# Kernel optimization log

Hardware: AMD Instinct MI355X
Metric: run time of the kernel (lower is better)

The kernel has to match this reference:

```python
import jax, jax.numpy as jnp
import numpy as np

BS = 2
EMBED = 256
NH = 8
NL = 4
NP = 4
HD = EMBED // NH
SHAPES = [(128, 128), (64, 64), (32, 32), (16, 16)]
NQ = sum(h * w for h, w in SHAPES)  # 21760


def setup_inputs() -> dict:
    key = jax.random.key(0)
    ks = jax.random.split(key, 12)
    s = 1.0 / np.sqrt(EMBED)
    return {
        "query": jax.random.normal(ks[0], (BS, NQ, EMBED), jnp.float32),
        "reference_points": jax.random.uniform(ks[1], (BS, NQ, NL, 2), jnp.float32),
        "value": jax.random.normal(ks[2], (BS, NQ, EMBED), jnp.float32),
        "W_off": jax.random.normal(ks[3], (EMBED, NH * NL * NP * 2), jnp.float32) * 0.01,
        "b_off": jax.random.normal(ks[4], (NH * NL * NP * 2,), jnp.float32) * 0.5,
        "W_attn": jax.random.normal(ks[5], (EMBED, NH * NL * NP), jnp.float32) * 0.02,
        "b_attn": jnp.zeros((NH * NL * NP,), jnp.float32),
        "W_v": jax.random.normal(ks[6], (EMBED, EMBED), jnp.float32) * s,
        "b_v": jnp.zeros((EMBED,), jnp.float32),
        "W_out": jax.random.normal(ks[7], (EMBED, EMBED), jnp.float32) * s,
        "b_out": jnp.zeros((EMBED,), jnp.float32),
        "value_spatial_shapes": np.asarray(SHAPES, dtype=np.int64),
    }


def _ms_deform_attn(value, shapes, loc, aw):
    # value: [bs,V,nh,d]; loc: [bs,nq,nh,L,P,2] in [0,1]; aw: [bs,nq,nh,L,P]
    bs, V, nh, d = value.shape
    nq = loc.shape[1]
    out = jnp.zeros((bs, nq, nh, d), value.dtype)
    start = 0
    b_idx = jnp.arange(bs)[:, None, None, None]
    h_idx = jnp.arange(nh)[None, None, :, None]
    for l, (H, W) in enumerate(shapes):
        H, W = int(H), int(W)
        v = value[:, start:start + H * W].reshape(bs, H, W, nh, d)
        start += H * W
        g = 2.0 * loc[:, :, :, l] - 1.0  # [bs,nq,nh,P,2], grid_sample convention
        # align_corners=False pixel coordinates
        x = ((g[..., 0] + 1.0) * W - 1.0) * 0.5
        y = ((g[..., 1] + 1.0) * H - 1.0) * 0.5
        x0 = jnp.floor(x); y0 = jnp.floor(y)
        wx1 = x - x0; wx0 = 1.0 - wx1
        wy1 = y - y0; wy0 = 1.0 - wy1

        def gather(yi, xi):
            inb = (yi >= 0) & (yi < H) & (xi >= 0) & (xi < W)
            yc = jnp.clip(yi, 0, H - 1).astype(jnp.int32)
            xc = jnp.clip(xi, 0, W - 1).astype(jnp.int32)
            vals = v[b_idx, yc, xc, h_idx]  # [bs,nq,nh,P,d]
            return vals * inb[..., None].astype(v.dtype)

        samp = (gather(y0, x0) * (wy0 * wx0)[..., None]
                + gather(y0, x0 + 1) * (wy0 * wx1)[..., None]
                + gather(y0 + 1, x0) * (wy1 * wx0)[..., None]
                + gather(y0 + 1, x0 + 1) * (wy1 * wx1)[..., None])
        out = out + jnp.einsum('bqhpd,bqhp->bqhd', samp, aw[:, :, :, l])
    return out.reshape(bs, nq, nh * d)


def reference(query, reference_points, value, W_off, b_off, W_attn, b_attn,
              W_v, b_v, W_out, b_out, value_spatial_shapes):
    shapes = np.asarray(value_spatial_shapes)  # static [L,2]
    bs, nq, _ = query.shape
    v = (value @ W_v + b_v).reshape(bs, -1, NH, HD)
    off = (query @ W_off + b_off).reshape(bs, nq, NH, NL, NP, 2)
    aw = (query @ W_attn + b_attn).reshape(bs, nq, NH, NL * NP)
    aw = jax.nn.softmax(aw, axis=-1).reshape(bs, nq, NH, NL, NP)
    # offset normalizer: (W,H) per level
    norm = jnp.asarray(shapes[:, ::-1].astype(np.float32))  # [L,2]
    loc = reference_points[:, :, None, :, None, :] + off / norm[None, None, None, :, None, :]
    out = _ms_deform_attn(v, shapes, loc, aw)
    return out @ W_out + b_out
```

## Files before the change

### kernel.cpp

```cpp
#include <hip/hip_runtime.h>
#include <math.h>

#define BS 2
#define NQ 21760
#define V_LEN 21760
#define EMBED 256
#define NH 8
#define NL 4
#define NP 4
#define HD 32

typedef __bf16 bf16;
typedef __bf16 bf16x8 __attribute__((ext_vector_type(8)));
typedef __bf16 bf16x4 __attribute__((ext_vector_type(4)));
typedef float f32x4 __attribute__((ext_vector_type(4)));
typedef float f32x2 __attribute__((ext_vector_type(2)));
typedef unsigned int u32;

#define GLOAD_LDS16(gp, lp_) \
    __builtin_amdgcn_global_load_lds( \
        (const __attribute__((address_space(1))) unsigned int*)(gp), \
        (__attribute__((address_space(3))) unsigned int*)(lp_), 16, 0, 0)

__global__ __launch_bounds__(256) void cast_all(
    const float* __restrict__ W_v, const float* __restrict__ W_off,
    const float* __restrict__ W_attn, const float* __restrict__ W_out,
    const float* __restrict__ b_off, const float* __restrict__ b_attn,
    bf16* __restrict__ WTv, bf16* __restrict__ WToa, bf16* __restrict__ WTu,
    float* __restrict__ bcat)
{
    const int bid = blockIdx.x;
    const int tid = threadIdx.x;
    if (bid == 56) {
        if (tid < 384) bcat[tid] = (tid < 256) ? b_off[tid] : b_attn[tid - 256];
        return;
    }
    const float* W; bf16* WT; int N, tile;
    if (bid < 16)      { W = W_v;    WT = WTv;           N = 256; tile = bid; }
    else if (bid < 32) { W = W_off;  WT = WToa;          N = 256; tile = bid - 16; }
    else if (bid < 40) { W = W_attn; WT = WToa + 65536;  N = 128; tile = bid - 32; }
    else               { W = W_out;  WT = WTu;           N = 256; tile = bid - 40; }
    const int ntn = N >> 6;
    const int k0 = (tile / ntn) * 64, n0 = (tile % ntn) * 64;

    __shared__ float lds[64][65];
    const int c = tid & 63, r4 = tid >> 6;
    #pragma unroll
    for (int p = 0; p < 16; p++) {
        int rr = r4 + p * 4;
        lds[rr][c] = W[(size_t)(k0 + rr) * N + n0 + c];
    }
    __syncthreads();
    #pragma unroll
    for (int p = 0; p < 16; p++) {
        int i = r4 + p * 4;
        WT[(size_t)(n0 + i) * 256 + k0 + c] = (bf16)lds[c][i];
    }
}

template<bool A_F32, bool OUT_BF16>
__global__ __launch_bounds__(256) void gemm_mfma(
    const void* __restrict__ Av, const bf16* __restrict__ WT,
    const float* __restrict__ bias, void* __restrict__ Cv,
    int N, int K, int ntn)
{
    const int nmt = gridDim.x / ntn;
    const int bmt = blockIdx.x % nmt;
    const int bnt = blockIdx.x / nmt;
    const int bm = bmt * 128, bn = bnt * 128;

    __shared__ __align__(16) bf16 Bs[2][128 * 32];
    __shared__ __align__(16) unsigned char AsRaw[2][A_F32 ? 128 * 32 * 4
                                                         : 128 * 32 * 2];

    const int tid = threadIdx.x;
    const int lane = tid & 63, wv = tid >> 6;
    const int wr = wv >> 1, wc = wv & 1;
    const int quad = lane >> 4, l16 = lane & 15;

    f32x4 acc[4][4];
    #pragma unroll
    for (int i = 0; i < 4; i++)
        #pragma unroll
        for (int j = 0; j < 4; j++)
            acc[i][j] = (f32x4){0.f, 0.f, 0.f, 0.f};

    const int b_row = tid >> 2, b_chunk = tid & 3;
    const int a_row8 = tid >> 3, a_phys = tid & 7;
    constexpr int NB = A_F32 ? 6 : 4;

    auto stage = [&](int buf, int k0) {
        if constexpr (A_F32) {
            const float* A = (const float*)Av;
            #pragma unroll
            for (int p = 0; p < 4; p++) {
                int row = a_row8 + p * 32;
                int csrc = a_phys ^ (row & 7);
                GLOAD_LDS16(&A[(size_t)(bm + row) * K + k0 + csrc * 4],
                            &AsRaw[buf][p * 4096 + tid * 16]);
            }
        } else {
            const bf16* A = (const bf16*)Av;
            #pragma unroll
            for (int p = 0; p < 2; p++) {
                int row = b_row + p * 64;
                GLOAD_LDS16(&A[(size_t)(bm + row) * K + k0 + b_chunk * 8],
                            &AsRaw[buf][p * 4096 + tid * 16]);
            }
        }
        #pragma unroll
        for (int p = 0; p < 2; p++) {
            int row = b_row + p * 64;
            GLOAD_LDS16(&WT[(size_t)(bn + row) * K + k0 + b_chunk * 8],
                        (unsigned char*)&Bs[buf][0] + p * 4096 + tid * 16);
        }
    };

    const int nt = K >> 5;
    stage(0, 0);
    int cur = 0;
    for (int t = 0; t < nt; t++) {
        __builtin_amdgcn_s_barrier();
        if (t + 1 < nt) {
            stage(cur ^ 1, (t + 1) << 5);
            asm volatile("s_waitcnt vmcnt(%0)" :: "n"(NB) : "memory");
        } else {
            asm volatile("s_waitcnt vmcnt(0)" ::: "memory");
        }
        __builtin_amdgcn_s_barrier();

        bf16x8 af[4], bfr[4];
        if constexpr (A_F32) {
            const float* Asf = (const float*)&AsRaw[cur][0];
            #pragma unroll
            for (int mi = 0; mi < 4; mi++) {
                int r = wr * 64 + mi * 16 + l16;
                int g = r & 7;
                f32x4 u0 = *(const f32x4*)&Asf[r * 32 + ((2 * quad) ^ g) * 4];
                f32x4 u1 = *(const f32x4*)&Asf[r * 32 + ((2 * quad + 1) ^ g) * 4];
                bf16x8 hh;
                hh[0] = (bf16)u0[0]; hh[1] = (bf16)u0[1]; hh[2] = (bf16)u0[2]; hh[3] = (bf16)u0[3];
                hh[4] = (bf16)u1[0]; hh[5] = (bf16)u1[1]; hh[6] = (bf16)u1[2]; hh[7] = (bf16)u1[3];
                af[mi] = hh;
            }
        } else {
            const bf16* Asb = (const bf16*)&AsRaw[cur][0];
            #pragma unroll
            for (int mi = 0; mi < 4; mi++) {
                int r = wr * 64 + mi * 16 + l16;
                af[mi] = *(const bf16x8*)&Asb[r * 32 + quad * 8];
            }
        }
        #pragma unroll
        for (int ni = 0; ni < 4; ni++) {
            int r = wc * 64 + ni * 16 + l16;
            bfr[ni] = *(const bf16x8*)&Bs[cur][r * 32 + quad * 8];
        }
        #pragma unroll
        for (int mi = 0; mi < 4; mi++)
            #pragma unroll
            for (int ni = 0; ni < 4; ni++)
                acc[mi][ni] = __builtin_amdgcn_mfma_f32_16x16x32_bf16(
                    af[mi], bfr[ni], acc[mi][ni], 0, 0, 0);
        cur ^= 1;
    }

    #pragma unroll
    for (int mi = 0; mi < 4; mi++) {
        #pragma unroll
        for (int ni = 0; ni < 4; ni++) {
            const int col = bn + wc * 64 + ni * 16 + l16;
            const int row0 = bm + wr * 64 + mi * 16 + quad * 4;
            const float bc = bias[col];
            #pragma unroll
            for (int r = 0; r < 4; r++) {
                float v = acc[mi][ni][r] + bc;
                if constexpr (OUT_BF16)
                    ((bf16*)Cv)[(size_t)(row0 + r) * N + col] = (bf16)v;
                else
                    ((float*)Cv)[(size_t)(row0 + r) * N + col] = v;
            }
        }
    }
}

__global__ __launch_bounds__(256) void deform_sample(
    const bf16* __restrict__ vproj, const float* __restrict__ offaw,
    const float* __restrict__ refp, bf16* __restrict__ sampled)
{
    const int wv = threadIdx.x >> 6;
    const int t = threadIdx.x & 63;
    const int q = blockIdx.x * 4 + wv;
    const int b = blockIdx.y;
    const int bq = b * NQ + q;

    __shared__ __align__(16) float s_w[4][128][4];
    __shared__ __align__(16) int   s_idx[4][128][4];

    const float* row = offaw + (size_t)bq * 384;

    const int hp = t & 7, e = t >> 3;
    float l0 = row[256 + hp * 16 + e];
    float l1 = row[256 + hp * 16 + e + 8];
    float m = fmaxf(l0, l1);
    m = fmaxf(m, __shfl_xor(m, 8));
    m = fmaxf(m, __shfl_xor(m, 16));
    m = fmaxf(m, __shfl_xor(m, 32));
    float e0 = __expf(l0 - m), e1 = __expf(l1 - m);
    float ssum = e0 + e1;
    ssum += __shfl_xor(ssum, 8);
    ssum += __shfl_xor(ssum, 16);
    ssum += __shfl_xor(ssum, 32);
    float rs = 1.0f / ssum;
    float awv[2] = {e0 * rs, e1 * rs};

    #pragma unroll
    for (int sI = 0; sI < 2; sI++) {
        int lp = e + sI * 8;
        int l = lp >> 2;
        int Wl = 128 >> l, Hl = 128 >> l;
        int st = (l == 0) ? 0 : (l == 1) ? 16384 : (l == 2) ? 20480 : 21504;
        float2 rp = *(const float2*)&refp[((size_t)bq * 4 + l) * 2];
        float2 oxy = *(const float2*)&row[hp * 32 + lp * 2];
        float fW = (float)Wl, fH = (float)Hl;
        float x = (rp.x + oxy.x / fW) * fW - 0.5f;
        float y = (rp.y + oxy.y / fH) * fH - 0.5f;
        float xf = floorf(x), yf = floorf(y);
        int x0 = (int)xf, y0 = (int)yf;
        float wx1 = x - xf, wx0 = 1.f - wx1;
        float wy1 = y - yf, wy0 = 1.f - wy1;
        float aw = awv[sI];
        bool vx0 = (x0 >= 0) && (x0 < Wl);
        bool vx1 = (x0 + 1 >= 0) && (x0 + 1 < Wl);
        bool vy0 = (y0 >= 0) && (y0 < Hl);
        bool vy1 = (y0 + 1 >= 0) && (y0 + 1 < Hl);
        int cx0 = min(max(x0, 0), Wl - 1), cx1 = min(max(x0 + 1, 0), Wl - 1);
        int cy0 = min(max(y0, 0), Hl - 1), cy1 = min(max(y0 + 1, 0), Hl - 1);
        int d = lp * 8 + hp;
        s_idx[wv][d][0] = st + cy0 * Wl + cx0;  s_w[wv][d][0] = (vy0 && vx0) ? wy0 * wx0 * aw : 0.f;
        s_idx[wv][d][1] = st + cy0 * Wl + cx1;  s_w[wv][d][1] = (vy0 && vx1) ? wy0 * wx1 * aw : 0.f;
        s_idx[wv][d][2] = st + cy1 * Wl + cx0;  s_w[wv][d][2] = (vy1 && vx0) ? wy1 * wx0 * aw : 0.f;
        s_idx[wv][d][3] = st + cy1 * Wl + cx1;  s_w[wv][d][3] = (vy1 && vx1) ? wy1 * wx1 * aw : 0.f;
    }
    __syncthreads();

    const int half = t >> 5;
    const int hg = (t & 31) >> 2;
    const int cg = t & 3;
    const int choff = hg * 32 + cg * 8;
    const bf16* vbc = vproj + (size_t)b * V_LEN * EMBED + choff;

    f32x2 a01 = {0.f, 0.f}, a23 = {0.f, 0.f}, a45 = {0.f, 0.f}, a67 = {0.f, 0.f};
    #pragma unroll
    for (int lpp = 0; lpp < 8; lpp++) {
        const int d = (lpp + 8 * half) * 8 + hg;
        const float4 w4 = *(const float4*)&s_w[wv][d][0];
        const int4  i4 = *(const int4*)&s_idx[wv][d][0];
        uint4 r0 = *(const uint4*)(vbc + ((size_t)i4.x << 8));
        uint4 r1 = *(const uint4*)(vbc + ((size_t)i4.y << 8));
        uint4 r2 = *(const uint4*)(vbc + ((size_t)i4.z << 8));
        uint4 r3 = *(const uint4*)(vbc + ((size_t)i4.w << 8));
        f32x2 v;
        #define ACC8(rr, ww) \
            v[0] = __uint_as_float((rr).x << 16); v[1] = __uint_as_float((rr).x & 0xFFFF0000u); a01 += v * (ww); \
            v[0] = __uint_as_float((rr).y << 16); v[1] = __uint_as_float((rr).y & 0xFFFF0000u); a23 += v * (ww); \
            v[0] = __uint_as_float((rr).z << 16); v[1] = __uint_as_float((rr).z & 0xFFFF0000u); a45 += v * (ww); \
            v[0] = __uint_as_float((rr).w << 16); v[1] = __uint_as_float((rr).w & 0xFFFF0000u); a67 += v * (ww);
        ACC8(r0, w4.x)
        ACC8(r1, w4.y)
        ACC8(r2, w4.z)
        ACC8(r3, w4.w)
        #undef ACC8
    }

    float s[8] = {a01[0], a01[1], a23[0], a23[1], a45[0], a45[1], a67[0], a67[1]};
    #pragma unroll
    for (int i = 0; i < 8; i++) s[i] += __shfl_xor(s[i], 32);

    if (t < 32) {
        bf16x8 o;
        #pragma unroll
        for (int i = 0; i < 8; i++) o[i] = (bf16)s[i];
        *(bf16x8*)&sampled[(size_t)bq * 256 + choff] = o;
    }
}

extern "C" void kernel_launch(void* const* d_in, const int* in_sizes, int n_in,
                              void* d_out, int out_size, void* d_ws, size_t ws_size,
                              hipStream_t stream)
{
    const float* query  = (const float*)d_in[0];
    const float* refp   = (const float*)d_in[1];
    const float* value  = (const float*)d_in[2];
    const float* W_off  = (const float*)d_in[3];
    const float* b_off  = (const float*)d_in[4];
    const float* W_attn = (const float*)d_in[5];
    const float* b_attn = (const float*)d_in[6];
    const float* W_v    = (const float*)d_in[7];
    const float* b_v    = (const float*)d_in[8];
    const float* W_out  = (const float*)d_in[9];
    const float* b_out  = (const float*)d_in[10];
    float* out = (float*)d_out;

    const int M = BS * NQ;

    char* ws = (char*)d_ws;
    bf16*  WTv   = (bf16*)ws;                      ws += 256 * 256 * 2;
    bf16*  WToa  = (bf16*)ws;                      ws += 384 * 256 * 2;
    bf16*  WTu   = (bf16*)ws;                      ws += 256 * 256 * 2;
    float* bcat  = (float*)ws;                     ws += 384 * 4;
    bf16*  vproj = (bf16*)ws;                      ws += (size_t)M * 256 * 2;
    float* offaw = (float*)ws;                     ws += (size_t)M * 384 * 4;
    bf16*  samp  = (bf16*)ws;                      ws += (size_t)M * 256 * 2;

    cast_all<<<57, 256, 0, stream>>>(W_v, W_off, W_attn, W_out, b_off, b_attn,
                                     WTv, WToa, WTu, bcat);

    gemm_mfma<true, true><<<(M / 128) * 2, 256, 0, stream>>>(value, WTv, b_v, vproj, 256, 256, 2);
    gemm_mfma<true, false><<<(M / 128) * 3, 256, 0, stream>>>(query, WToa, bcat, offaw, 384, 256, 3);
    deform_sample<<<dim3(NQ / 4, BS), dim3(256), 0, stream>>>(vproj, offaw, refp, samp);
    gemm_mfma<false, false><<<(M / 128) * 2, 256, 0, stream>>>(samp, WTu, b_out, out, 256, 256, 2);
}
```

Before: 293.3 us.

## Store projected value head-major and fetch bilinear corner pairs as contiguous rows

The value-projection GEMM now writes its bf16 output in a [batch, head, V_LEN, 32] layout, so that horizontally adjacent pixels of one head sit next to each other in memory. The sampling kernel clamps each corner pair to a single base index. It folds the out-of-bounds and clamping logic into four recomputed weights. Each lane then loads two 16-byte chunks, the top and bottom rows, which together span 64 contiguous bytes for the x0/x1 pair, instead of four scattered loads per point. Lane roles are remapped so lanes 0-3 and 4-7 cover the two x neighbours, and their partial sums are reduced with a shuffle. The costs are scattered 2-byte stores in the GEMM epilogue and more index arithmetic.

Measured after the change: 283.5 us. 3.3% less time.

```diff
diff --git a/kernel.cpp b/kernel.cpp
--- a/kernel.cpp
+++ b/kernel.cpp
@@ -58,7 +58,7 @@
     }
 }
 
-template<bool A_F32, bool OUT_BF16>
+template<bool A_F32, int OUT_MODE>
 __global__ __launch_bounds__(256) void gemm_mfma(
     const void* __restrict__ Av, const bf16* __restrict__ WT,
     const float* __restrict__ bias, void* __restrict__ Cv,
@@ -175,13 +175,30 @@
             #pragma unroll
             for (int r = 0; r < 4; r++) {
                 float v = acc[mi][ni][r] + bc;
-                if constexpr (OUT_BF16)
+                if constexpr (OUT_MODE == 0) {
+                    ((float*)Cv)[(size_t)(row0 + r) * N + col] = v;
+                } else if constexpr (OUT_MODE == 1) {
                     ((bf16*)Cv)[(size_t)(row0 + r) * N + col] = (bf16)v;
-                else
-                    ((float*)Cv)[(size_t)(row0 + r) * N + col] = v;
-            }
-        }
-    }
+                } else {
+                    int rv = row0 + r;
+                    int bb = (rv >= V_LEN) ? 1 : 0;
+                    int vv = rv - bb * V_LEN;
+                    ((bf16*)Cv)[((size_t)(bb * NH + (col >> 5)) * V_LEN + vv) * 32
+                                + (col & 31)] = (bf16)v;
+                }
+            }
+        }
+    }
+}
+
+__device__ inline void acc8(const uint4& rr, float ww,
+                            f32x2& a01, f32x2& a23, f32x2& a45, f32x2& a67)
+{
+    f32x2 v;
+    v[0] = __uint_as_float(rr.x << 16); v[1] = __uint_as_float(rr.x & 0xFFFF0000u); a01 += v * ww;
+    v[0] = __uint_as_float(rr.y << 16); v[1] = __uint_as_float(rr.y & 0xFFFF0000u); a23 += v * ww;
+    v[0] = __uint_as_float(rr.z << 16); v[1] = __uint_as_float(rr.z & 0xFFFF0000u); a45 += v * ww;
+    v[0] = __uint_as_float(rr.w << 16); v[1] = __uint_as_float(rr.w & 0xFFFF0000u); a67 += v * ww;
 }
 
 __global__ __launch_bounds__(256) void deform_sample(
@@ -195,7 +212,7 @@
     const int bq = b * NQ + q;
 
     __shared__ __align__(16) float s_w[4][128][4];
-    __shared__ __align__(16) int   s_idx[4][128][4];
+    __shared__ __align__(16) int   s_idx[4][128];
 
     const float* row = offaw + (size_t)bq * 384;
 
@@ -230,58 +247,55 @@
         float wx1 = x - xf, wx0 = 1.f - wx1;
         float wy1 = y - yf, wy0 = 1.f - wy1;
         float aw = awv[sI];
-        bool vx0 = (x0 >= 0) && (x0 < Wl);
-        bool vx1 = (x0 + 1 >= 0) && (x0 + 1 < Wl);
-        bool vy0 = (y0 >= 0) && (y0 < Hl);
-        bool vy1 = (y0 + 1 >= 0) && (y0 + 1 < Hl);
+        float wx0p = ((x0 >= 0) && (x0 < Wl)) ? wx0 : 0.f;
+        float wx1p = ((x0 + 1 >= 0) && (x0 + 1 < Wl)) ? wx1 : 0.f;
+        float wy0p = ((y0 >= 0) && (y0 < Hl)) ? wy0 : 0.f;
+        float wy1p = ((y0 + 1 >= 0) && (y0 + 1 < Hl)) ? wy1 : 0.f;
+        int px = min(max(x0, 0), Wl - 2), py = min(max(y0, 0), Hl - 2);
         int cx0 = min(max(x0, 0), Wl - 1), cx1 = min(max(x0 + 1, 0), Wl - 1);
         int cy0 = min(max(y0, 0), Hl - 1), cy1 = min(max(y0 + 1, 0), Hl - 1);
+        float sx0 = ((cx0 == px) ? wx0p : 0.f) + ((cx1 == px) ? wx1p : 0.f);
+        float sx1 = ((cx0 == px + 1) ? wx0p : 0.f) + ((cx1 == px + 1) ? wx1p : 0.f);
+        float sy0 = ((cy0 == py) ? wy0p : 0.f) + ((cy1 == py) ? wy1p : 0.f);
+        float sy1 = ((cy0 == py + 1) ? wy0p : 0.f) + ((cy1 == py + 1) ? wy1p : 0.f);
         int d = lp * 8 + hp;
-        s_idx[wv][d][0] = st + cy0 * Wl + cx0;  s_w[wv][d][0] = (vy0 && vx0) ? wy0 * wx0 * aw : 0.f;
-        s_idx[wv][d][1] = st + cy0 * Wl + cx1;  s_w[wv][d][1] = (vy0 && vx1) ? wy0 * wx1 * aw : 0.f;
-        s_idx[wv][d][2] = st + cy1 * Wl + cx0;  s_w[wv][d][2] = (vy1 && vx0) ? wy1 * wx0 * aw : 0.f;
-        s_idx[wv][d][3] = st + cy1 * Wl + cx1;  s_w[wv][d][3] = (vy1 && vx1) ? wy1 * wx1 * aw : 0.f;
+        s_idx[wv][d] = st + py * Wl + px;
+        s_w[wv][d][0] = sy0 * sx0 * aw;
+        s_w[wv][d][1] = sy0 * sx1 * aw;
+        s_w[wv][d][2] = sy1 * sx0 * aw;
+        s_w[wv][d][3] = sy1 * sx1 * aw;
     }
     __syncthreads();
 
-    const int half = t >> 5;
-    const int hg = (t & 31) >> 2;
-    const int cg = t & 3;
-    const int choff = hg * 32 + cg * 8;
-    const bf16* vbc = vproj + (size_t)b * V_LEN * EMBED + choff;
+    const int h = t >> 3, j = t & 7;
+    const bf16* vb = vproj + ((size_t)(b * NH + h) * V_LEN) * 32 + j * 8;
 
     f32x2 a01 = {0.f, 0.f}, a23 = {0.f, 0.f}, a45 = {0.f, 0.f}, a67 = {0.f, 0.f};
     #pragma unroll
-    for (int lpp = 0; lpp < 8; lpp++) {
-        const int d = (lpp + 8 * half) * 8 + hg;
+    for (int lp = 0; lp < 16; lp++) {
+        const int Wl = 128 >> (lp >> 2);
+        const int d = lp * 8 + h;
+        const int base = s_idx[wv][d];
         const float4 w4 = *(const float4*)&s_w[wv][d][0];
-        const int4  i4 = *(const int4*)&s_idx[wv][d][0];
-        uint4 r0 = *(const uint4*)(vbc + ((size_t)i4.x << 8));
-        uint4 r1 = *(const uint4*)(vbc + ((size_t)i4.y << 8));
-        uint4 r2 = *(const uint4*)(vbc + ((size_t)i4.z << 8));
-        uint4 r3 = *(const uint4*)(vbc + ((size_t)i4.w << 8));
-        f32x2 v;
-        #define ACC8(rr, ww) \
-            v[0] = __uint_as_float((rr).x << 16); v[1] = __uint_as_float((rr).x & 0xFFFF0000u); a01 += v * (ww); \
-            v[0] = __uint_as_float((rr).y << 16); v[1] = __uint_as_float((rr).y & 0xFFFF0000u); a23 += v * (ww); \
-            v[0] = __uint_as_float((rr).z << 16); v[1] = __uint_as_float((rr).z & 0xFFFF0000u); a45 += v * (ww); \
-            v[0] = __uint_as_float((rr).w << 16); v[1] = __uint_as_float((rr).w & 0xFFFF0000u); a67 += v * (ww);
-        ACC8(r0, w4.x)
-        ACC8(r1, w4.y)
-        ACC8(r2, w4.z)
-        ACC8(r3, w4.w)
-        #undef ACC8
+        const bf16* p0 = vb + (size_t)base * 32;
+        uint4 r0 = *(const uint4*)p0;
+        uint4 r1 = *(const uint4*)(p0 + Wl * 32);
+        const bool xs = (j & 4) != 0;
+        float wA = xs ? w4.y : w4.x;
+        float wB = xs ? w4.w : w4.z;
+        acc8(r0, wA, a01, a23, a45, a67);
+        acc8(r1, wB, a01, a23, a45, a67);
     }
 
     float s[8] = {a01[0], a01[1], a23[0], a23[1], a45[0], a45[1], a67[0], a67[1]};
     #pragma unroll
-    for (int i = 0; i < 8; i++) s[i] += __shfl_xor(s[i], 32);
-
-    if (t < 32) {
+    for (int i = 0; i < 8; i++) s[i] += __shfl_xor(s[i], 4);
+
+    if ((t & 4) == 0) {
         bf16x8 o;
         #pragma unroll
         for (int i = 0; i < 8; i++) o[i] = (bf16)s[i];
-        *(bf16x8*)&sampled[(size_t)bq * 256 + choff] = o;
+        *(bf16x8*)&sampled[(size_t)bq * 256 + h * 32 + (t & 3) * 8] = o;
     }
 }
 
@@ -316,8 +330,8 @@
     cast_all<<<57, 256, 0, stream>>>(W_v, W_off, W_attn, W_out, b_off, b_attn,
                                      WTv, WToa, WTu, bcat);
 
-    gemm_mfma<true, true><<<(M / 128) * 2, 256, 0, stream>>>(value, WTv, b_v, vproj, 256, 256, 2);
-    gemm_mfma<true, false><<<(M / 128) * 3, 256, 0, stream>>>(query, WToa, bcat, offaw, 384, 256, 3);
+    gemm_mfma<true, 2><<<(M / 128) * 2, 256, 0, stream>>>(value, WTv, b_v, vproj, 256, 256, 2);
+    gemm_mfma<true, 0><<<(M / 128) * 3, 256, 0, stream>>>(query, WToa, bcat, offaw, 384, 256, 3);
     deform_sample<<<dim3(NQ / 4, BS), dim3(256), 0, stream>>>(vproj, offaw, refp, samp);
-    gemm_mfma<false, false><<<(M / 128) * 2, 256, 0, stream>>>(samp, WTu, b_out, out, 256, 256, 2);
-}
+    gemm_mfma<false, 0><<<(M / 128) * 2, 256, 0, stream>>>(samp, WTu, b_out, out, 256, 256, 2);
+}
```
